# Performance work log

Measured on AMD Instinct MI355X. Metric: run time of the kernel, lower is better.

## Reference

```python
import jax, jax.numpy as jnp
from jax import lax
import numpy as np

B, T, E, H, ENC, V = 64, 49, 512, 512, 1024, 32000


def setup_inputs() -> dict:
    key = jax.random.key(0)
    ks = jax.random.split(key, 12)
    embeddings = jax.random.normal(ks[0], (B, T, E), jnp.float32)
    encoder_out = jax.random.normal(ks[1], (B, ENC), jnp.float32)
    # caption lengths sorted descending (module assumes this for ragged truncation)
    lens = jax.random.randint(ks[2], (B,), 10, T + 2)
    caption_lengths = jnp.sort(lens)[::-1]
    caption_lengths = caption_lengths.at[0].set(T + 1)  # max decode length == T
    s = 1.0 / np.sqrt(H)
    u = lambda k, shp, lim: jax.random.uniform(k, shp, jnp.float32, -lim, lim)
    W_ih = u(ks[3], (4 * H, E), s)
    W_hh = u(ks[4], (4 * H, H), s)
    b_ih = u(ks[5], (4 * H,), s)
    b_hh = u(ks[6], (4 * H,), s)
    se = 1.0 / np.sqrt(ENC)
    W_init_h = u(ks[7], (H, ENC), se)
    b_init_h = u(ks[8], (H,), se)
    W_init_c = u(ks[9], (H, ENC), se)
    b_init_c = u(ks[10], (H,), se)
    W_fc = u(ks[11], (V, H), 0.1)  # init_weights: uniform(-0.1, 0.1)
    b_fc = jnp.zeros((V,), jnp.float32)
    return dict(embeddings=embeddings, encoder_out=encoder_out,
                caption_lengths=caption_lengths,
                W_ih=W_ih, W_hh=W_hh, b_ih=b_ih, b_hh=b_hh,
                W_init_h=W_init_h, b_init_h=b_init_h,
                W_init_c=W_init_c, b_init_c=b_init_c,
                W_fc=W_fc, b_fc=b_fc)


def reference(embeddings, encoder_out, caption_lengths,
              W_ih, W_hh, b_ih, b_hh,
              W_init_h, b_init_h, W_init_c, b_init_c,
              W_fc, b_fc):
    # dropout is treated as identity (eval mode) for the deterministic reference
    h0 = encoder_out @ W_init_h.T + b_init_h  # [B, H]
    c0 = encoder_out @ W_init_c.T + b_init_c
    decode_lengths = caption_lengths - 1
    Tn = embeddings.shape[1]
    # mask[t, b] = True iff example b is still active at step t
    mask = jnp.arange(Tn)[:, None] < decode_lengths[None, :]  # [T, B]
    xs = jnp.transpose(embeddings, (1, 0, 2))  # [T, B, E]

    def step(carry, inp):
        h, c = carry
        x, m = inp
        gates = x @ W_ih.T + b_ih + h @ W_hh.T + b_hh  # [B, 4H]
        i, f, g, o = jnp.split(gates, 4, axis=-1)
        i = jax.nn.sigmoid(i); f = jax.nn.sigmoid(f)
        g = jnp.tanh(g); o = jax.nn.sigmoid(o)
        c_new = f * c + i * g
        h_new = o * jnp.tanh(c_new)
        preds = h_new @ W_fc.T + b_fc  # [B, V]
        m2 = m[:, None]
        # inactive rows: state frozen (torch only updates h[:batch_size_t]),
        # predictions stay zero
        h = jnp.where(m2, h_new, h)
        c = jnp.where(m2, c_new, c)
        preds = jnp.where(m2, preds, 0.0)
        return (h, c), preds

    (_, _), preds = lax.scan(step, (h0, c0), (xs, mask))
    predictions = jnp.transpose(preds, (1, 0, 2))  # [B, T, V]
    return predictions, decode_lengths
```

## Files before the change

### kernel.cpp

```cpp
#include <hip/hip_runtime.h>
#include <stdint.h>

#define B_    64
#define T_    49
#define E_    512
#define H_    512
#define ENC_  1024
#define V_    32000
#define G4_   2048
#define M_    3136
#define MPAD_ 3200
#define NPROD 32
#define NWG   512
#define NTN   250

typedef __attribute__((ext_vector_type(8))) short bf16x8;
typedef __attribute__((ext_vector_type(4))) float f32x4;

static __device__ __forceinline__ unsigned short f2bf(float f) {
  union { float f; uint32_t u; } v; v.f = f;
  uint32_t r = v.u + 0x7FFFu + ((v.u >> 16) & 1u);
  return (unsigned short)(r >> 16);
}

static __device__ __forceinline__ void async16(const void* g, void* lds) {
  __builtin_amdgcn_global_load_lds(
      (const __attribute__((address_space(1))) unsigned int*)g,
      (__attribute__((address_space(3))) unsigned int*)lds, 16, 0, 0);
}

static __device__ __forceinline__ float sigf(float x) { return 1.0f / (1.0f + expf(-x)); }

__global__ __launch_bounds__(256) void convert_kernel(
    const float* __restrict__ Wih, const float* __restrict__ Whh,
    const float* __restrict__ emb,
    unsigned short* __restrict__ WihB, unsigned short* __restrict__ WhhB,
    unsigned short* __restrict__ AxB) {
  const int n_wih = (G4_ * E_) / 4;
  const int n_whh = (G4_ * H_) / 4;
  const int n_emb = (B_ * T_ * E_) / 4;
  const int n_pad = ((MPAD_ - M_) * E_) / 4;
  const long total = (long)n_wih + n_whh + n_emb + n_pad;
  for (long u = (long)blockIdx.x * blockDim.x + threadIdx.x; u < total;
       u += (long)gridDim.x * blockDim.x) {
    long i = u;
    if (i < n_wih) {
      float4 v = ((const float4*)Wih)[i];
      ushort4 o; o.x = f2bf(v.x); o.y = f2bf(v.y); o.z = f2bf(v.z); o.w = f2bf(v.w);
      ((ushort4*)WihB)[i] = o; continue;
    }
    i -= n_wih;
    if (i < n_whh) {
      float4 v = ((const float4*)Whh)[i];
      ushort4 o; o.x = f2bf(v.x); o.y = f2bf(v.y); o.z = f2bf(v.z); o.w = f2bf(v.w);
      ((ushort4*)WhhB)[i] = o; continue;
    }
    i -= n_whh;
    if (i < n_emb) {
      int bt = (int)(i >> 7);
      int e4 = (int)(i & 127);
      int b = bt / T_, t = bt - b * T_;
      float4 v = ((const float4*)emb)[i];
      ushort4 o; o.x = f2bf(v.x); o.y = f2bf(v.y); o.z = f2bf(v.z); o.w = f2bf(v.w);
      ((ushort4*)AxB)[((long)(t * 64 + b) << 7) + e4] = o; continue;
    }
    i -= n_emb;
    ushort4 z; z.x = z.y = z.z = z.w = 0;
    ((ushort4*)AxB)[((long)M_ << 7) + i] = z;
  }
}

__global__ __launch_bounds__(256) void init_kernel(
    const float* __restrict__ enc, const int* __restrict__ cap,
    const float* __restrict__ Wh, const float* __restrict__ bh,
    const float* __restrict__ Wc, const float* __restrict__ bc,
    unsigned short* __restrict__ h0b, float* __restrict__ c0,
    float* __restrict__ out_dl, int* __restrict__ meta,
    int* __restrict__ rowmap, int* __restrict__ zrowmap) {
  __shared__ __align__(16) float e[ENC_];
  __shared__ int s_nb[T_];
  __shared__ int s_start[T_ + 1];
  const int b = blockIdx.x, q = blockIdx.y, tid = threadIdx.x;
  ((float4*)e)[tid] = ((const float4*)(enc + (size_t)b * ENC_))[tid];
  __syncthreads();
  const bool is_c = tid >= 128;
  const int j = q * 128 + (tid & 127);
  const float* W = is_c ? Wc : Wh;
  float s = is_c ? bc[j] : bh[j];
  const float4* wr = (const float4*)(W + (size_t)j * ENC_);
  const float4* e4 = (const float4*)e;
#pragma unroll 4
  for (int k = 0; k < ENC_ / 4; ++k) {
    float4 w = wr[k], v = e4[k];
    s += w.x * v.x + w.y * v.y + w.z * v.z + w.w * v.w;
  }
  if (is_c) c0[(size_t)b * H_ + j] = s;
  else      h0b[(size_t)b * H_ + j] = f2bf(s);
  if (b == 0 && q == 0 && tid < B_) out_dl[tid] = (float)(cap[tid] - 1);

  if (b == 0 && q == 0) {
    __syncthreads();
    if (tid < T_) {
      int cnt = 0;
      for (int bb = 0; bb < B_; ++bb) cnt += (cap[bb] - 1 > tid) ? 1 : 0;
      s_nb[tid] = cnt;
    }
    __syncthreads();
    if (tid == 0) {
      int acc = 0;
      for (int t = 0; t < T_; ++t) { s_start[t] = acc; acc += s_nb[t]; }
      s_start[T_] = acc;
      const int Mc = acc;
      const int MT = (Mc + 127) >> 7;
      meta[100] = Mc;
      meta[101] = MT;
      meta[104] = M_ - Mc;
      meta[105] = NTN + (M_ - Mc) + MT * NTN;
      for (int i = Mc; i < MT * 128; ++i) rowmap[i] = -1;
    }
    __syncthreads();
    if (tid < T_) {
      meta[tid] = s_start[tid];
      const int st = s_start[tid], nb = s_nb[tid];
      for (int bb = 0; bb < nb; ++bb) rowmap[st + bb] = bb * T_ + tid;
      int zst = 0;
      for (int t2 = 0; t2 < tid; ++t2) zst += B_ - s_nb[t2];
      for (int bb = nb; bb < B_; ++bb) zrowmap[zst + (bb - nb)] = bb * T_ + tid;
    }
    __syncthreads();
    if (tid < 26) {
      const int Mc = s_start[T_];
      const int MT = (Mc + 127) >> 7;
      if (tid < MT) {
        int last = tid * 128 + 127;
        if (last > Mc - 1) last = Mc - 1;
        int tlast = 0;
        for (int t2 = 0; t2 < T_; ++t2) if (s_start[t2] <= last) tlast = t2;
        meta[110 + tid] = tlast + 1;
      }
    }
  }
}

__global__ __launch_bounds__(256) void pad_kernel(const int* __restrict__ meta,
                                                  unsigned short* __restrict__ Hall) {
  const int Mc = meta[100], MT = meta[101];
  const int tot = (MT * 128 - Mc) * 64;
  for (int i = blockIdx.x * blockDim.x + threadIdx.x; i < tot;
       i += gridDim.x * blockDim.x) {
    const int row = Mc + (i >> 6), c = i & 63;
    ushort4 z; z.x = z.y = z.z = z.w = 0;
    *(ushort4*)((char*)Hall + (size_t)row * 1024 + c * 16) = z;
  }
}

__global__ __launch_bounds__(256) void gemm_gx(
    const unsigned short* __restrict__ A, const unsigned short* __restrict__ Bm,
    float* __restrict__ C, const float* __restrict__ bias0, const float* __restrict__ bias1) {
  __shared__ __align__(16) char smem[65536];
  const int tid = threadIdx.x, lane = tid & 63, wid = tid >> 6;
  const int nt = blockIdx.x, mt = blockIdx.y;
  const int wr = wid >> 1, wc = wid & 1;
  const int m0 = mt * 128, n0 = nt * 128;
  f32x4 acc[4][4] = {};

  auto stage = [&](int buf, int kit) {
    const int k0b = kit * 128;
#pragma unroll
    for (int i = 0; i < 4; ++i) {
      int chunk = wid * 4 + i;
      int d = chunk * 1024 + lane * 16;
      int row = d >> 7, colb = d & 127;
      int sc = colb ^ ((row & 7) << 4);
      async16((const char*)A + (size_t)(m0 + row) * 1024 + k0b + sc,
              smem + buf * 16384 + chunk * 1024);
      async16((const char*)Bm + (size_t)(n0 + row) * 1024 + k0b + sc,
              smem + 32768 + buf * 16384 + chunk * 1024);
    }
  };

  stage(0, 0);
  __syncthreads();
  for (int kit = 0; kit < 8; ++kit) {
    const int buf = kit & 1;
    if (kit < 7) stage(buf ^ 1, kit + 1);
    const char* Ab = smem + buf * 16384;
    const char* Bb = smem + 32768 + buf * 16384;
#pragma unroll
    for (int kb = 0; kb < 2; ++kb) {
      const int colb = kb * 64 + (lane >> 4) * 16;
      bf16x8 af[4], bfb[4];
#pragma unroll
      for (int rt = 0; rt < 4; ++rt) {
        int ar = wr * 64 + rt * 16 + (lane & 15);
        af[rt] = *(const bf16x8*)(Ab + ar * 128 + (colb ^ ((ar & 7) << 4)));
        int br = wc * 64 + rt * 16 + (lane & 15);
        bfb[rt] = *(const bf16x8*)(Bb + br * 128 + (colb ^ ((br & 7) << 4)));
      }
#pragma unroll
      for (int i = 0; i < 4; ++i)
#pragma unroll
        for (int j = 0; j < 4; ++j)
          acc[i][j] = __builtin_amdgcn_mfma_f32_16x16x32_bf16(af[i], bfb[j], acc[i][j], 0, 0, 0);
    }
    __syncthreads();
  }
#pragma unroll
  for (int i = 0; i < 4; ++i) {
    const int rbase = m0 + wr * 64 + i * 16 + (lane >> 4) * 4;
#pragma unroll
    for (int j = 0; j < 4; ++j) {
      const int col = n0 + wc * 64 + j * 16 + (lane & 15);
#pragma unroll
      for (int r = 0; r < 4; ++r)
        C[(size_t)(rbase + r) * G4_ + col] = acc[i][j][r] + bias0[col] + bias1[col];
    }
  }
}

__global__ __launch_bounds__(256) void fused_kernel(
    const float* __restrict__ Gx, const unsigned short* __restrict__ WhhB,
    const unsigned short* __restrict__ h0b, const float* __restrict__ c0,
    unsigned short* __restrict__ hsl, unsigned short* __restrict__ Hall,
    const float* __restrict__ Wfc, unsigned short* __restrict__ WfcB,
    const float* __restrict__ bfc, const int* __restrict__ cap,
    float* __restrict__ outp, int* __restrict__ ctrl, const int* __restrict__ meta,
    const int* __restrict__ rowmap, const int* __restrict__ zrowmap) {
  __shared__ __align__(16) char smem[65536];
  const int tid = threadIdx.x, lane = tid & 63, g = tid >> 6;
  int* s_tile = (int*)(smem + 65532);
  int* s_role = (int*)(smem + 65528);

  {
    int xcc;
    asm volatile("s_getreg_b32 %0, hwreg(HW_REG_XCC_ID)" : "=s"(xcc));
    if (tid == 0) {
      xcc &= 7;
      int a = __hip_atomic_fetch_add(&ctrl[592 + xcc * 16], 1, __ATOMIC_RELAXED,
                                     __HIP_MEMORY_SCOPE_AGENT);
      if (a == NPROD - 1) {
        int expected = 0;
        __hip_atomic_compare_exchange_strong(&ctrl[560], &expected, xcc + 1,
                                             __ATOMIC_RELAXED, __ATOMIC_RELAXED,
                                             __HIP_MEMORY_SCOPE_AGENT);
      }
      int e;
      for (;;) {
        e = __hip_atomic_load(&ctrl[560], __ATOMIC_RELAXED, __HIP_MEMORY_SCOPE_AGENT);
        if (e) break;
        __builtin_amdgcn_s_sleep(2);
      }
      int slot = NPROD;
      if (e - 1 == xcc)
        slot = __hip_atomic_fetch_add(&ctrl[576], 1, __ATOMIC_RELAXED,
                                      __HIP_MEMORY_SCOPE_AGENT);
      *s_role = slot;
    }
    __syncthreads();
  }
  const int w = *s_role;
  __syncthreads();

  if (w < NPROD) {
    __builtin_amdgcn_s_setprio(1);
    const int hc0 = w * 16;
    const int gcol = g * 512 + hc0 + (lane & 15);
    const int ko = (lane >> 4) * 8;
    bf16x8 wf[16];
#pragma unroll
    for (int kb = 0; kb < 16; ++kb)
      wf[kb] = *(const bf16x8*)&WhhB[(size_t)gcol * 512 + kb * 32 + ko];
    const int b = tid >> 2, hq = (tid & 3) * 4, hc = hc0 + hq;
    const int dl = cap[b] - 1;
    f32x4 creg = *(const f32x4*)&c0[b * H_ + hc];
    ushort4 hold = *(const ushort4*)&h0b[b * H_ + hc];
    const int myoff = ((b * 32) ^ (((b >> 2) & 7) << 4) ^ ((hq >> 3) << 4)) + ((hq & 7) * 2);
    {
      union { ushort4 s; unsigned long long u; } cv; cv.s = hold;
      *(unsigned long long*)((char*)hsl + w * 2048 + myoff) = cv.u;
    }
    int arb[4];
#pragma unroll
    for (int rt = 0; rt < 4; ++rt) {
      int ar = rt * 16 + (lane & 15);
      arb[rt] = (ar * 32) ^ (((ar >> 2) & 7) << 4) ^ (((lane >> 4) & 1) << 4);
    }
    const int chunk_hi = lane >> 5;
    float (*gl)[64][16] = (float (*)[64][16])smem;
    asm volatile("s_waitcnt vmcnt(0)" ::: "memory");
    __syncthreads();
    if (tid == 0)
      __hip_atomic_store(&ctrl[w * 16], 1, __ATOMIC_RELAXED, __HIP_MEMORY_SCOPE_AGENT);

    for (int t = 0; t < T_; ++t) {
      const size_t gxr = ((size_t)t * 64 + b) * (size_t)G4_ + hc;
      f32x4 xi = *(const f32x4*)&Gx[gxr + 0];
      f32x4 xf = *(const f32x4*)&Gx[gxr + 512];
      f32x4 xg = *(const f32x4*)&Gx[gxr + 1024];
      f32x4 xo = *(const f32x4*)&Gx[gxr + 1536];
      __builtin_amdgcn_sched_barrier(0);
      if (tid < 64) {
        const int need = t + 1;
        for (;;) {
          int v = (lane < NPROD)
                      ? __hip_atomic_load(&ctrl[lane * 16], __ATOMIC_RELAXED, __HIP_MEMORY_SCOPE_AGENT)
                      : need;
          if (__all(v >= need)) break;
          __builtin_amdgcn_s_sleep(1);
        }
        if (tid == 0 && w == 0 && t > 0)
          __hip_atomic_store(&ctrl[512], t, __ATOMIC_RELAXED, __HIP_MEMORY_SCOPE_AGENT);
      }
      __syncthreads();
      {
        const char* src = (const char*)hsl + (t & 1) * 65536 + g * 16384 + lane * 16;
        char* dst = smem + g * 16384 + lane * 16;
        int4 hv[16];
#pragma unroll
        for (int i = 0; i < 16; ++i)
          asm volatile("global_load_dwordx4 %0, %1, off sc0"
                       : "=&v"(hv[i]) : "v"(src + i * 1024));
        asm volatile("s_waitcnt vmcnt(0)" ::: "memory");
#pragma unroll
        for (int i = 0; i < 16; ++i)
          *(int4*)(dst + i * 1024) = hv[i];
      }
      __syncthreads();
      f32x4 accp[4] = {};
#pragma unroll
      for (int kb = 0; kb < 16; ++kb) {
        const int cbase = (kb * 2 + chunk_hi) * 2048;
#pragma unroll
        for (int rt = 0; rt < 4; ++rt) {
          bf16x8 af = *(const bf16x8*)(smem + cbase + arb[rt]);
          accp[rt] = __builtin_amdgcn_mfma_f32_16x16x32_bf16(af, wf[kb], accp[rt], 0, 0, 0);
        }
      }
      __syncthreads();
#pragma unroll
      for (int rt = 0; rt < 4; ++rt)
#pragma unroll
        for (int r = 0; r < 4; ++r)
          gl[g][rt * 16 + (lane >> 4) * 4 + r][lane & 15] = accp[rt][r];
      __syncthreads();
      f32x4 vi = xi + *(const f32x4*)&gl[0][b][hq];
      f32x4 vf = xf + *(const f32x4*)&gl[1][b][hq];
      f32x4 vg = xg + *(const f32x4*)&gl[2][b][hq];
      f32x4 vo = xo + *(const f32x4*)&gl[3][b][hq];
      f32x4 cn;
      ushort4 hb16;
      {
        float hv4[4];
#pragma unroll
        for (int k = 0; k < 4; ++k) {
          float iv = sigf(vi[k]), fv = sigf(vf[k]), gv = tanhf(vg[k]), ov = sigf(vo[k]);
          cn[k] = fv * creg[k] + iv * gv;
          hv4[k] = ov * tanhf(cn[k]);
        }
        hb16.x = f2bf(hv4[0]); hb16.y = f2bf(hv4[1]); hb16.z = f2bf(hv4[2]); hb16.w = f2bf(hv4[3]);
      }
      if (t < dl) {
        union { ushort4 s; unsigned long long u; } cv; cv.s = hb16;
        __hip_atomic_store((unsigned long long*)&Hall[((size_t)(meta[t] + b)) * H_ + hc],
                           cv.u, __ATOMIC_RELAXED, __HIP_MEMORY_SCOPE_AGENT);
        hold = hb16; creg = cn;
      }
      if (t + 1 < T_) {
        union { ushort4 s; unsigned long long u; } cv; cv.s = hold;
        *(unsigned long long*)((char*)hsl + ((t + 1) & 1) * 65536 + w * 2048 + myoff) = cv.u;
      }
      asm volatile("s_waitcnt vmcnt(0)" ::: "memory");
      __syncthreads();
      if (tid == 0)
        __hip_atomic_store(&ctrl[w * 16], t + 2, __ATOMIC_RELAXED, __HIP_MEMORY_SCOPE_AGENT);
    }
    if (w == 0 && tid < 64) {
      const int need = T_ + 1;
      for (;;) {
        int v = (lane < NPROD)
                    ? __hip_atomic_load(&ctrl[lane * 16], __ATOMIC_RELAXED, __HIP_MEMORY_SCOPE_AGENT)
                    : need;
        if (__all(v >= need)) break;
        __builtin_amdgcn_s_sleep(1);
      }
      if (tid == 0)
        __hip_atomic_store(&ctrl[512], T_, __ATOMIC_RELAXED, __HIP_MEMORY_SCOPE_AGENT);
    }
    __builtin_amdgcn_s_setprio(0);
  }

  const int NZI = meta[104];
  const int NTOT = meta[105];
  const int wid = tid >> 6;
  const int wr = wid >> 1, wc = wid & 1;
  for (;;) {
    __syncthreads();
    if (tid == 0)
      *s_tile = __hip_atomic_fetch_add(&ctrl[528], 1, __ATOMIC_RELAXED, __HIP_MEMORY_SCOPE_AGENT);
    __syncthreads();
    const int tile = *s_tile;
    __syncthreads();
    if (tile >= NTOT) break;

    if (tile < NTN) {
      const float4* src = (const float4*)(Wfc + (size_t)tile * 128 * 512);
      unsigned long long* dst = (unsigned long long*)WfcB + (size_t)tile * 16384;
      for (int i = tid; i < 16384; i += 256) {
        float4 v = src[i];
        union { ushort4 s; unsigned long long u; } cv;
        cv.s.x = f2bf(v.x); cv.s.y = f2bf(v.y); cv.s.z = f2bf(v.z); cv.s.w = f2bf(v.w);
        __hip_atomic_store(&dst[i], cv.u, __ATOMIC_RELAXED, __HIP_MEMORY_SCOPE_AGENT);
      }
      asm volatile("s_waitcnt vmcnt(0)" ::: "memory");
      __syncthreads();
      if (tid == 0)
        __hip_atomic_fetch_add(&ctrl[544], 1, __ATOMIC_RELAXED, __HIP_MEMORY_SCOPE_AGENT);
      continue;
    }

    if (tile < NTN + NZI) {
      const int bt = zrowmap[tile - NTN];
      f32x4* dst = (f32x4*)(outp + (size_t)bt * V_);
      f32x4 z = {0.0f, 0.0f, 0.0f, 0.0f};
      for (int i = tid; i < V_ / 4; i += 256) dst[i] = z;
      continue;
    }

    const int gt = tile - NTN - NZI;
    const int mt = gt / NTN, nt = gt - mt * NTN;
    const int m0 = mt * 128, n0 = nt * 128;
    const int need = meta[110 + mt];
    if (tid == 0) {
      while (__hip_atomic_load(&ctrl[544], __ATOMIC_RELAXED, __HIP_MEMORY_SCOPE_AGENT) < NTN)
        __builtin_amdgcn_s_sleep(2);
      while (__hip_atomic_load(&ctrl[512], __ATOMIC_RELAXED, __HIP_MEMORY_SCOPE_AGENT) < need)
        __builtin_amdgcn_s_sleep(8);
    }
    __syncthreads();

    f32x4 acc[4][4] = {};
    auto stage = [&](int buf, int kit) {
      const int k0b = kit * 128;
#pragma unroll
      for (int i = 0; i < 4; ++i) {
        int chunk = wid * 4 + i;
        int d = chunk * 1024 + lane * 16;
        int row = d >> 7, colb = d & 127;
        int sc = colb ^ ((row & 7) << 4);
        async16((const char*)Hall + (size_t)(m0 + row) * 1024 + k0b + sc,
                smem + buf * 16384 + chunk * 1024);
        async16((const char*)WfcB + (size_t)(n0 + row) * 1024 + k0b + sc,
                smem + 32768 + buf * 16384 + chunk * 1024);
      }
    };
    stage(0, 0);
    __syncthreads();
    for (int kit = 0; kit < 8; ++kit) {
      const int buf = kit & 1;
      if (kit < 7) stage(buf ^ 1, kit + 1);
      const char* Ab = smem + buf * 16384;
      const char* Bb = smem + 32768 + buf * 16384;
#pragma unroll
      for (int kb = 0; kb < 2; ++kb) {
        const int colb = kb * 64 + (lane >> 4) * 16;
        bf16x8 af[4], bfb[4];
#pragma unroll
        for (int rt = 0; rt < 4; ++rt) {
          int ar = wr * 64 + rt * 16 + (lane & 15);
          af[rt] = *(const bf16x8*)(Ab + ar * 128 + (colb ^ ((ar & 7) << 4)));
          int br = wc * 64 + rt * 16 + (lane & 15);
          bfb[rt] = *(const bf16x8*)(Bb + br * 128 + (colb ^ ((br & 7) << 4)));
        }
#pragma unroll
        for (int i = 0; i < 4; ++i)
#pragma unroll
          for (int j = 0; j < 4; ++j)
            acc[i][j] = __builtin_amdgcn_mfma_f32_16x16x32_bf16(af[i], bfb[j], acc[i][j], 0, 0, 0);
      }
      __syncthreads();
    }
    float* Ct = (float*)smem;
#pragma unroll
    for (int j = 0; j < 4; ++j) {
      const int colL = wc * 64 + j * 16 + (lane & 15);
      const float bz = bfc[n0 + colL];
#pragma unroll
      for (int i = 0; i < 4; ++i) {
        const int rb = wr * 64 + i * 16 + (lane >> 4) * 4;
#pragma unroll
        for (int r = 0; r < 4; ++r) {
          const int row = rb + r;
          Ct[row * 128 + (colL ^ ((row & 7) << 2))] = acc[i][j][r] + bz;
        }
      }
    }
    __syncthreads();
    const int c4 = tid & 31;
    const int rsub = tid >> 5;
#pragma unroll
    for (int itr = 0; itr < 16; ++itr) {
      const int row = itr * 8 + rsub;
      const int bt = rowmap[m0 + row];
      if (bt < 0) continue;
      f32x4 v = *(const f32x4*)&Ct[row * 128 + ((c4 ^ (row & 7)) << 2)];
      *(f32x4*)(outp + (size_t)bt * V_ + n0 + (c4 << 2)) = v;
    }
  }
}

extern "C" void kernel_launch(void* const* d_in, const int* in_sizes, int n_in,
                              void* d_out, int out_size, void* d_ws, size_t ws_size,
                              hipStream_t stream) {
  const float* emb = (const float*)d_in[0];
  const float* enc = (const float*)d_in[1];
  const int*   cap = (const int*)d_in[2];
  const float* Wih = (const float*)d_in[3];
  const float* Whh = (const float*)d_in[4];
  const float* bih = (const float*)d_in[5];
  const float* bhh = (const float*)d_in[6];
  const float* Wh0 = (const float*)d_in[7];
  const float* bh0 = (const float*)d_in[8];
  const float* Wc0 = (const float*)d_in[9];
  const float* bc0 = (const float*)d_in[10];
  const float* Wfc = (const float*)d_in[11];
  const float* bfc = (const float*)d_in[12];
  float* out = (float*)d_out;

  char* ws = (char*)d_ws;
  size_t o = 0;
  auto carve = [&](size_t bytes) { void* p = ws + o; o += (bytes + 255) & ~(size_t)255; return p; };
  unsigned short* WihB = (unsigned short*)carve((size_t)G4_ * E_ * 2);
  unsigned short* WhhB = (unsigned short*)carve((size_t)G4_ * H_ * 2);
  unsigned short* WfcB = (unsigned short*)carve((size_t)V_ * H_ * 2);
  unsigned short* AxB  = (unsigned short*)carve((size_t)MPAD_ * E_ * 2);
  float*          Gx   = (float*)carve((size_t)MPAD_ * G4_ * 4);
  unsigned short* Hall = (unsigned short*)carve((size_t)MPAD_ * H_ * 2);
  unsigned short* h0b  = (unsigned short*)carve((size_t)B_ * H_ * 2);
  float*          cst  = (float*)carve((size_t)B_ * H_ * 4);
  unsigned short* hsl  = (unsigned short*)carve((size_t)2 * 65536);
  int*            ctrl = (int*)carve(4096);
  int*            meta = (int*)carve(1024);
  int*            rowmap = (int*)carve((size_t)MPAD_ * 4);
  int*            zrowmap = (int*)carve((size_t)MPAD_ * 4);
  (void)ws_size; (void)in_sizes; (void)n_in; (void)out_size;

  hipMemsetAsync(ctrl, 0, 4096, stream);
  convert_kernel<<<dim3(1024), dim3(256), 0, stream>>>(Wih, Whh, emb, WihB, WhhB, AxB);
  init_kernel<<<dim3(64, 4), dim3(256), 0, stream>>>(enc, cap, Wh0, bh0, Wc0, bc0, h0b, cst,
                                                     out + (size_t)B_ * T_ * V_,
                                                     meta, rowmap, zrowmap);
  pad_kernel<<<dim3(32), dim3(256), 0, stream>>>(meta, Hall);
  gemm_gx<<<dim3(G4_ / 128, MPAD_ / 128), dim3(256), 0, stream>>>(AxB, WihB, Gx, bih, bhh);
  fused_kernel<<<dim3(NWG), dim3(256), 0, stream>>>(Gx, WhhB, h0b, cst, hsl, Hall,
                                                    Wfc, WfcB, bfc, cap, out, ctrl,
                                                    meta, rowmap, zrowmap);
}
```

Before: 397.4 us.

## Use 512-thread workgroups with 128KB LDS in fused LSTM/FC kernel

Halves the fused kernel's grid to 256 workgroups and doubles each to 512 threads, one per CU with 128KB of shared memory. The recurrent producer path keeps its 256-thread compute on the first half of the threads, while all 512 threads share the h-state staging copy. The FC GEMM consumer tiles are re-split across 8 waves (2x4 layout, 64x32 per wave) so each wave holds fewer accumulators. The aim is fewer resident workgroups and fewer accumulator registers per wave; the risk is idle waves on the producer path and a different occupancy balance.

```diff
diff --git a/kernel.cpp b/kernel.cpp
--- a/kernel.cpp
+++ b/kernel.cpp
@@ -11,7 +11,7 @@
 #define M_    3136
 #define MPAD_ 3200
 #define NPROD 32
-#define NWG   512
+#define NWG   256
 #define NTN   250
 
 typedef __attribute__((ext_vector_type(8))) short bf16x8;
@@ -218,7 +218,7 @@
   }
 }
 
-__global__ __launch_bounds__(256) void fused_kernel(
+__global__ __launch_bounds__(512, 1) void fused_kernel(
     const float* __restrict__ Gx, const unsigned short* __restrict__ WhhB,
     const unsigned short* __restrict__ h0b, const float* __restrict__ c0,
     unsigned short* __restrict__ hsl, unsigned short* __restrict__ Hall,
@@ -226,10 +226,10 @@
     const float* __restrict__ bfc, const int* __restrict__ cap,
     float* __restrict__ outp, int* __restrict__ ctrl, const int* __restrict__ meta,
     const int* __restrict__ rowmap, const int* __restrict__ zrowmap) {
-  __shared__ __align__(16) char smem[65536];
-  const int tid = threadIdx.x, lane = tid & 63, g = tid >> 6;
-  int* s_tile = (int*)(smem + 65532);
-  int* s_role = (int*)(smem + 65528);
+  __shared__ __align__(16) char smem[131072];
+  const int tid = threadIdx.x, lane = tid & 63, wid = tid >> 6;
+  int* s_tile = (int*)(smem + 131068);
+  int* s_role = (int*)(smem + 131064);
 
   {
     int xcc;
@@ -264,40 +264,48 @@
   if (w < NPROD) {
     __builtin_amdgcn_s_setprio(1);
     const int hc0 = w * 16;
-    const int gcol = g * 512 + hc0 + (lane & 15);
-    const int ko = (lane >> 4) * 8;
+    const bool act = tid < 256;
+    const int g = wid;
+    const int chunk_hi = lane >> 5;
     bf16x8 wf[16];
-#pragma unroll
-    for (int kb = 0; kb < 16; ++kb)
-      wf[kb] = *(const bf16x8*)&WhhB[(size_t)gcol * 512 + kb * 32 + ko];
-    const int b = tid >> 2, hq = (tid & 3) * 4, hc = hc0 + hq;
-    const int dl = cap[b] - 1;
-    f32x4 creg = *(const f32x4*)&c0[b * H_ + hc];
-    ushort4 hold = *(const ushort4*)&h0b[b * H_ + hc];
-    const int myoff = ((b * 32) ^ (((b >> 2) & 7) << 4) ^ ((hq >> 3) << 4)) + ((hq & 7) * 2);
-    {
+    f32x4 creg = {};
+    ushort4 hold = {};
+    int b = 0, hq = 0, hc = 0, dl = 0, myoff = 0;
+    int arb[4] = {};
+    if (act) {
+      const int gcol = g * 512 + hc0 + (lane & 15);
+      const int ko = (lane >> 4) * 8;
+#pragma unroll
+      for (int kb = 0; kb < 16; ++kb)
+        wf[kb] = *(const bf16x8*)&WhhB[(size_t)gcol * 512 + kb * 32 + ko];
+      b = tid >> 2; hq = (tid & 3) * 4; hc = hc0 + hq;
+      dl = cap[b] - 1;
+      creg = *(const f32x4*)&c0[b * H_ + hc];
+      hold = *(const ushort4*)&h0b[b * H_ + hc];
+      myoff = ((b * 32) ^ (((b >> 2) & 7) << 4) ^ ((hq >> 3) << 4)) + ((hq & 7) * 2);
       union { ushort4 s; unsigned long long u; } cv; cv.s = hold;
       *(unsigned long long*)((char*)hsl + w * 2048 + myoff) = cv.u;
-    }
-    int arb[4];
-#pragma unroll
-    for (int rt = 0; rt < 4; ++rt) {
-      int ar = rt * 16 + (lane & 15);
-      arb[rt] = (ar * 32) ^ (((ar >> 2) & 7) << 4) ^ (((lane >> 4) & 1) << 4);
-    }
-    const int chunk_hi = lane >> 5;
-    float (*gl)[64][16] = (float (*)[64][16])smem;
+#pragma unroll
+      for (int rt = 0; rt < 4; ++rt) {
+        int ar = rt * 16 + (lane & 15);
+        arb[rt] = (ar * 32) ^ (((ar >> 2) & 7) << 4) ^ (((lane >> 4) & 1) << 4);
+      }
+    }
+    float (*gl)[64][16] = (float (*)[64][16])(smem + 65536);
     asm volatile("s_waitcnt vmcnt(0)" ::: "memory");
     __syncthreads();
     if (tid == 0)
       __hip_atomic_store(&ctrl[w * 16], 1, __ATOMIC_RELAXED, __HIP_MEMORY_SCOPE_AGENT);
 
     for (int t = 0; t < T_; ++t) {
-      const size_t gxr = ((size_t)t * 64 + b) * (size_t)G4_ + hc;
-      f32x4 xi = *(const f32x4*)&Gx[gxr + 0];
-      f32x4 xf = *(const f32x4*)&Gx[gxr + 512];
-      f32x4 xg = *(const f32x4*)&Gx[gxr + 1024];
-      f32x4 xo = *(const f32x4*)&Gx[gxr + 1536];
+      f32x4 xi = {}, xf = {}, xg = {}, xo = {};
+      if (act) {
+        const size_t gxr = ((size_t)t * 64 + b) * (size_t)G4_ + hc;
+        xi = *(const f32x4*)&Gx[gxr + 0];
+        xf = *(const f32x4*)&Gx[gxr + 512];
+        xg = *(const f32x4*)&Gx[gxr + 1024];
+        xo = *(const f32x4*)&Gx[gxr + 1536];
+      }
       __builtin_amdgcn_sched_barrier(0);
       if (tid < 64) {
         const int need = t + 1;
@@ -313,61 +321,64 @@
       }
       __syncthreads();
       {
-        const char* src = (const char*)hsl + (t & 1) * 65536 + g * 16384 + lane * 16;
-        char* dst = smem + g * 16384 + lane * 16;
-        int4 hv[16];
-#pragma unroll
-        for (int i = 0; i < 16; ++i)
+        const char* src = (const char*)hsl + (t & 1) * 65536 + tid * 16;
+        char* dst = smem + tid * 16;
+        int4 hv[8];
+#pragma unroll
+        for (int i = 0; i < 8; ++i)
           asm volatile("global_load_dwordx4 %0, %1, off sc0"
-                       : "=&v"(hv[i]) : "v"(src + i * 1024));
+                       : "=&v"(hv[i]) : "v"(src + i * 8192));
         asm volatile("s_waitcnt vmcnt(0)" ::: "memory");
 #pragma unroll
-        for (int i = 0; i < 16; ++i)
-          *(int4*)(dst + i * 1024) = hv[i];
+        for (int i = 0; i < 8; ++i)
+          *(int4*)(dst + i * 8192) = hv[i];
       }
       __syncthreads();
-      f32x4 accp[4] = {};
-#pragma unroll
-      for (int kb = 0; kb < 16; ++kb) {
-        const int cbase = (kb * 2 + chunk_hi) * 2048;
-#pragma unroll
-        for (int rt = 0; rt < 4; ++rt) {
-          bf16x8 af = *(const bf16x8*)(smem + cbase + arb[rt]);
-          accp[rt] = __builtin_amdgcn_mfma_f32_16x16x32_bf16(af, wf[kb], accp[rt], 0, 0, 0);
-        }
+      if (act) {
+        f32x4 accp[4] = {};
+#pragma unroll
+        for (int kb = 0; kb < 16; ++kb) {
+          const int cbase = (kb * 2 + chunk_hi) * 2048;
+#pragma unroll
+          for (int rt = 0; rt < 4; ++rt) {
+            bf16x8 af = *(const bf16x8*)(smem + cbase + arb[rt]);
+            accp[rt] = __builtin_amdgcn_mfma_f32_16x16x32_bf16(af, wf[kb], accp[rt], 0, 0, 0);
+          }
+        }
+#pragma unroll
+        for (int rt = 0; rt < 4; ++rt)
+#pragma unroll
+          for (int r = 0; r < 4; ++r)
+            gl[g][rt * 16 + (lane >> 4) * 4 + r][lane & 15] = accp[rt][r];
       }
       __syncthreads();
-#pragma unroll
-      for (int rt = 0; rt < 4; ++rt)
-#pragma unroll
-        for (int r = 0; r < 4; ++r)
-          gl[g][rt * 16 + (lane >> 4) * 4 + r][lane & 15] = accp[rt][r];
-      __syncthreads();
-      f32x4 vi = xi + *(const f32x4*)&gl[0][b][hq];
-      f32x4 vf = xf + *(const f32x4*)&gl[1][b][hq];
-      f32x4 vg = xg + *(const f32x4*)&gl[2][b][hq];
-      f32x4 vo = xo + *(const f32x4*)&gl[3][b][hq];
-      f32x4 cn;
-      ushort4 hb16;
-      {
-        float hv4[4];
-#pragma unroll
-        for (int k = 0; k < 4; ++k) {
-          float iv = sigf(vi[k]), fv = sigf(vf[k]), gv = tanhf(vg[k]), ov = sigf(vo[k]);
-          cn[k] = fv * creg[k] + iv * gv;
-          hv4[k] = ov * tanhf(cn[k]);
-        }
-        hb16.x = f2bf(hv4[0]); hb16.y = f2bf(hv4[1]); hb16.z = f2bf(hv4[2]); hb16.w = f2bf(hv4[3]);
-      }
-      if (t < dl) {
-        union { ushort4 s; unsigned long long u; } cv; cv.s = hb16;
-        __hip_atomic_store((unsigned long long*)&Hall[((size_t)(meta[t] + b)) * H_ + hc],
-                           cv.u, __ATOMIC_RELAXED, __HIP_MEMORY_SCOPE_AGENT);
-        hold = hb16; creg = cn;
-      }
-      if (t + 1 < T_) {
-        union { ushort4 s; unsigned long long u; } cv; cv.s = hold;
-        *(unsigned long long*)((char*)hsl + ((t + 1) & 1) * 65536 + w * 2048 + myoff) = cv.u;
+      if (act) {
+        f32x4 vi = xi + *(const f32x4*)&gl[0][b][hq];
+        f32x4 vf = xf + *(const f32x4*)&gl[1][b][hq];
+        f32x4 vg = xg + *(const f32x4*)&gl[2][b][hq];
+        f32x4 vo = xo + *(const f32x4*)&gl[3][b][hq];
+        f32x4 cn;
+        ushort4 hb16;
+        {
+          float hv4[4];
+#pragma unroll
+          for (int k = 0; k < 4; ++k) {
+            float iv = sigf(vi[k]), fv = sigf(vf[k]), gv = tanhf(vg[k]), ov = sigf(vo[k]);
+            cn[k] = fv * creg[k] + iv * gv;
+            hv4[k] = ov * tanhf(cn[k]);
+          }
+          hb16.x = f2bf(hv4[0]); hb16.y = f2bf(hv4[1]); hb16.z = f2bf(hv4[2]); hb16.w = f2bf(hv4[3]);
+        }
+        if (t < dl) {
+          union { ushort4 s; unsigned long long u; } cv; cv.s = hb16;
+          __hip_atomic_store((unsigned long long*)&Hall[((size_t)(meta[t] + b)) * H_ + hc],
+                             cv.u, __ATOMIC_RELAXED, __HIP_MEMORY_SCOPE_AGENT);
+          hold = hb16; creg = cn;
+        }
+        if (t + 1 < T_) {
+          union { ushort4 s; unsigned long long u; } cv; cv.s = hold;
+          *(unsigned long long*)((char*)hsl + ((t + 1) & 1) * 65536 + w * 2048 + myoff) = cv.u;
+        }
       }
       asm volatile("s_waitcnt vmcnt(0)" ::: "memory");
       __syncthreads();
@@ -391,8 +402,7 @@
 
   const int NZI = meta[104];
   const int NTOT = meta[105];
-  const int wid = tid >> 6;
-  const int wr = wid >> 1, wc = wid & 1;
+  const int wr = wid >> 2, wc = wid & 3;
   for (;;) {
     __syncthreads();
     if (tid == 0)
@@ -405,7 +415,7 @@
     if (tile < NTN) {
       const float4* src = (const float4*)(Wfc + (size_t)tile * 128 * 512);
       unsigned long long* dst = (unsigned long long*)WfcB + (size_t)tile * 16384;
-      for (int i = tid; i < 16384; i += 256) {
+      for (int i = tid; i < 16384; i += 512) {
         float4 v = src[i];
         union { ushort4 s; unsigned long long u; } cv;
         cv.s.x = f2bf(v.x); cv.s.y = f2bf(v.y); cv.s.z = f2bf(v.z); cv.s.w = f2bf(v.w);
@@ -422,7 +432,7 @@
       const int bt = zrowmap[tile - NTN];
       f32x4* dst = (f32x4*)(outp + (size_t)bt * V_);
       f32x4 z = {0.0f, 0.0f, 0.0f, 0.0f};
-      for (int i = tid; i < V_ / 4; i += 256) dst[i] = z;
+      for (int i = tid; i < V_ / 4; i += 512) dst[i] = z;
       continue;
     }
 
@@ -438,12 +448,12 @@
     }
     __syncthreads();
 
-    f32x4 acc[4][4] = {};
+    f32x4 acc[4][2] = {};
     auto stage = [&](int buf, int kit) {
       const int k0b = kit * 128;
 #pragma unroll
-      for (int i = 0; i < 4; ++i) {
-        int chunk = wid * 4 + i;
+      for (int i = 0; i < 2; ++i) {
+        int chunk = wid * 2 + i;
         int d = chunk * 1024 + lane * 16;
         int row = d >> 7, colb = d & 127;
         int sc = colb ^ ((row & 7) << 4);
@@ -463,34 +473,35 @@
 #pragma unroll
       for (int kb = 0; kb < 2; ++kb) {
         const int colb = kb * 64 + (lane >> 4) * 16;
-        bf16x8 af[4], bfb[4];
+        bf16x8 bfb[2];
+#pragma unroll
+        for (int j = 0; j < 2; ++j) {
+          int br = wc * 32 + j * 16 + (lane & 15);
+          bfb[j] = *(const bf16x8*)(Bb + br * 128 + (colb ^ ((br & 7) << 4)));
+        }
 #pragma unroll
         for (int rt = 0; rt < 4; ++rt) {
           int ar = wr * 64 + rt * 16 + (lane & 15);
-          af[rt] = *(const bf16x8*)(Ab + ar * 128 + (colb ^ ((ar & 7) << 4)));
-          int br = wc * 64 + rt * 16 + (lane & 15);
-          bfb[rt] = *(const bf16x8*)(Bb + br * 128 + (colb ^ ((br & 7) << 4)));
-        }
-#pragma unroll
-        for (int i = 0; i < 4; ++i)
-#pragma unroll
-          for (int j = 0; j < 4; ++j)
-            acc[i][j] = __builtin_amdgcn_mfma_f32_16x16x32_bf16(af[i], bfb[j], acc[i][j], 0, 0, 0);
+          bf16x8 af = *(const bf16x8*)(Ab + ar * 128 + (colb ^ ((ar & 7) << 4)));
+#pragma unroll
+          for (int j = 0; j < 2; ++j)
+            acc[rt][j] = __builtin_amdgcn_mfma_f32_16x16x32_bf16(af, bfb[j], acc[rt][j], 0, 0, 0);
+        }
       }
       __syncthreads();
     }
     float* Ct = (float*)smem;
 #pragma unroll
-    for (int j = 0; j < 4; ++j) {
-      const int colL = wc * 64 + j * 16 + (lane & 15);
+    for (int j = 0; j < 2; ++j) {
+      const int colL = wc * 32 + j * 16 + (lane & 15);
       const float bz = bfc[n0 + colL];
 #pragma unroll
-      for (int i = 0; i < 4; ++i) {
-        const int rb = wr * 64 + i * 16 + (lane >> 4) * 4;
+      for (int rt = 0; rt < 4; ++rt) {
+        const int rb = wr * 64 + rt * 16 + (lane >> 4) * 4;
 #pragma unroll
         for (int r = 0; r < 4; ++r) {
           const int row = rb + r;
-          Ct[row * 128 + (colL ^ ((row & 7) << 2))] = acc[i][j][r] + bz;
+          Ct[row * 128 + (colL ^ ((row & 7) << 2))] = acc[rt][j][r] + bz;
         }
       }
     }
@@ -498,8 +509,8 @@
     const int c4 = tid & 31;
     const int rsub = tid >> 5;
 #pragma unroll
-    for (int itr = 0; itr < 16; ++itr) {
-      const int row = itr * 8 + rsub;
+    for (int itr = 0; itr < 8; ++itr) {
+      const int row = itr * 16 + rsub;
       const int bt = rowmap[m0 + row];
       if (bt < 0) continue;
       f32x4 v = *(const f32x4*)&Ct[row * 128 + ((c4 ^ (row & 7)) << 2)];
@@ -551,7 +562,7 @@
                                                      meta, rowmap, zrowmap);
   pad_kernel<<<dim3(32), dim3(256), 0, stream>>>(meta, Hall);
   gemm_gx<<<dim3(G4_ / 128, MPAD_ / 128), dim3(256), 0, stream>>>(AxB, WihB, Gx, bih, bhh);
-  fused_kernel<<<dim3(NWG), dim3(256), 0, stream>>>(Gx, WhhB, h0b, cst, hsl, Hall,
+  fused_kernel<<<dim3(NWG), dim3(512), 0, stream>>>(Gx, WhhB, h0b, cst, hsl, Hall,
                                                     Wfc, WfcB, bfc, cap, out, ctrl,
                                                     meta, rowmap, zrowmap);
 }
```

Result: faster. 387.4 us (-2.5%).
